# Optimization experiments

Hardware: AMD Instinct MI355X
Metric: run time of the kernel (lower is better)

## Reference

```python
import jax, jax.numpy as jnp
import numpy as np

NUM_EMBEDDINGS = 8192
EMBEDDING_DIM = 512
BETA = 0.25


def setup_inputs() -> dict:
    key = jax.random.key(0)
    k1, k2 = jax.random.split(key)
    x = jax.random.normal(k1, (16, 1024, EMBEDDING_DIM), dtype=jnp.float32)
    # torch.nn.init.uniform_ -> U[0, 1)
    embeddings = jax.random.uniform(k2, (NUM_EMBEDDINGS, EMBEDDING_DIM), dtype=jnp.float32)
    return {"x": x, "embeddings": embeddings}


def reference(x, embeddings):
    input_shape = x.shape
    flat = x.reshape(-1, EMBEDDING_DIM)                      # [N, D]
    sim = jnp.matmul(flat, embeddings.T)                     # [N, K]
    s1 = jnp.sum(flat * flat, axis=1, keepdims=True)         # [N, 1]
    s2 = jnp.sum(embeddings * embeddings, axis=1)            # [K]
    distances = s1 + s2 - 2.0 * sim                          # [N, K]
    idx = jnp.argmin(distances, axis=1)                      # [N]
    # direct gather (math-equivalent to one-hot @ codebook)
    quantized = embeddings[idx].reshape(input_shape)
    sg = jax.lax.stop_gradient
    commitment_loss = BETA * jnp.mean((sg(quantized) - x) ** 2)
    codebook_loss = jnp.mean((quantized - sg(x)) ** 2)
    loss = commitment_loss + codebook_loss
    out = x + sg(quantized - x)                              # straight-through
    return (out, quantized, loss)
```

## Files before the change

kernel.cpp:

```cpp
#include <hip/hip_runtime.h>

#define DIM 512
#define N_ROWS 16384
#define K_CODES 8192
#define BK 32
#define TM 128
#define TN 128
#define NG (K_CODES / TN)
#define OUT_ELEMS (N_ROWS * DIM)
#define MARGIN 0.125f
#define CAP_ITEMS 262144
#define NT (DIM / BK)

typedef _Float16 f16;
typedef _Float16 f16x8 __attribute__((ext_vector_type(8)));
typedef float f32x4 __attribute__((ext_vector_type(4)));

__device__ __forceinline__ unsigned long long pack_di(float d, int i) {
  unsigned u = __float_as_uint(d);
  u = (u & 0x80000000u) ? ~u : (u | 0x80000000u);
  return ((unsigned long long)u << 32) | (unsigned)i;
}

__global__ __launch_bounds__(256) void vq_split_kernel(const float* __restrict__ src,
                                                       f16* __restrict__ x16) {
  int i = (blockIdx.x * 256 + threadIdx.x) * 8;
  float4 v0 = *(const float4*)(src + i);
  float4 v1 = *(const float4*)(src + i + 4);
  float f[8] = {v0.x, v0.y, v0.z, v0.w, v1.x, v1.y, v1.z, v1.w};
  f16x8 h;
  #pragma unroll
  for (int j = 0; j < 8; ++j) h[j] = (f16)f[j];
  *(f16x8*)(x16 + i) = h;
}

__global__ __launch_bounds__(256) void vq_split_enorm_kernel(
    const float* __restrict__ emb, f16* __restrict__ e16,
    float* __restrict__ enorm, int* __restrict__ rcounter) {
  int gid  = blockIdx.x * 256 + threadIdx.x;
  if (gid == 0) *rcounter = 0;
  int code = gid >> 6;
  int lane = gid & 63;
  size_t off = (size_t)code * DIM + lane * 8;
  float4 v0 = *(const float4*)(emb + off);
  float4 v1 = *(const float4*)(emb + off + 4);
  float f[8] = {v0.x, v0.y, v0.z, v0.w, v1.x, v1.y, v1.z, v1.w};
  f16x8 h;
  float s = 0.0f;
  #pragma unroll
  for (int j = 0; j < 8; ++j) {
    h[j] = (f16)f[j];
    s = fmaf(f[j], f[j], s);
  }
  *(f16x8*)(e16 + off) = h;
  #pragma unroll
  for (int o = 32; o > 0; o >>= 1) s += __shfl_down(s, o);
  if (lane == 0) enorm[code] = s;
}

__device__ __forceinline__ void gl2lds16(const f16* g, f16* l) {
  __builtin_amdgcn_global_load_lds((const __attribute__((address_space(1))) unsigned int*)g,
                                   (__attribute__((address_space(3))) unsigned int*)l,
                                   16, 0, 0);
}

__device__ __forceinline__ void top2_merge(float& d1, int& i1, float& d2,
                                           float od1, int oi1, float od2) {
  if (od1 < d1 || (od1 == d1 && oi1 < i1)) {
    d2 = fminf(d1, od2);
    d1 = od1; i1 = oi1;
  } else {
    d2 = fminf(d2, od1);
  }
}

__global__ __launch_bounds__(256, 4) void vq_argmin_mfma_kernel(
    const f16* __restrict__ x16, const f16* __restrict__ e16,
    const float* __restrict__ enorm,
    float* __restrict__ cand_d1, int* __restrict__ cand_i1, float* __restrict__ cand_d2) {
  __shared__ __align__(16) f16 Ax[2][TM * BK];
  __shared__ __align__(16) f16 Be[2][TN * BK];
  __shared__ float red_d1[2][TM];
  __shared__ int   red_i1[2][TM];
  __shared__ float red_d2[2][TM];

  const int tid  = threadIdx.x;
  const int wave = tid >> 6;
  const int lane = tid & 63;
  const int bm = blockIdx.x, bn = blockIdx.y;
  const int wr = (wave >> 1) * 64;
  const int wc = (wave & 1) * 64;

  const f16* gsrc0;
  int ldoff;
  {
    const int srow = lane >> 2;
    const int scg  = ((lane & 3) ^ ((lane >> 3) & 3)) * 8;
    const int rowoff = (wave & 1) * 64;
    if (wave < 2) { gsrc0 = x16 + (size_t)(bm * TM + rowoff + srow) * DIM + scg; }
    else          { gsrc0 = e16 + (size_t)(bn * TN + rowoff + srow) * DIM + scg; }
    ldoff = rowoff * BK;
  }
  f16* dstA0 = (wave < 2) ? &Ax[0][ldoff] : &Be[0][ldoff];
  f16* dstA1 = (wave < 2) ? &Ax[1][ldoff] : &Be[1][ldoff];

  f32x4 acc[4][4];
  #pragma unroll
  for (int i = 0; i < 4; ++i)
    #pragma unroll
    for (int j = 0; j < 4; ++j)
      acc[i][j] = (f32x4){0.f, 0.f, 0.f, 0.f};

  const int fr = lane & 15;
  const int fq = lane >> 4;
  const int sw8 = (fq ^ ((fr >> 1) & 3)) * 8;

  #pragma unroll
  for (int i = 0; i < 4; ++i)
    gl2lds16(gsrc0 + (size_t)(16 * i) * DIM, dstA0 + (16 * i) * BK);
  __syncthreads();

  #pragma unroll 2
  for (int s = 0; s < NT; ++s) {
    const int cur = s & 1;
    if (s + 1 < NT) {
      f16* nb = cur ? dstA0 : dstA1;
      const int k1 = (s + 1) * BK;
      #pragma unroll
      for (int i = 0; i < 4; ++i)
        gl2lds16(gsrc0 + (size_t)(16 * i) * DIM + k1, nb + (16 * i) * BK);
    }

    const f16* A = cur ? &Ax[1][0] : &Ax[0][0];
    const f16* B = cur ? &Be[1][0] : &Be[0][0];
    f16x8 a[4], b[4];
    #pragma unroll
    for (int f = 0; f < 4; ++f) {
      a[f] = *(const f16x8*)&A[(wr + f * 16 + fr) * BK + sw8];
      b[f] = *(const f16x8*)&B[(wc + f * 16 + fr) * BK + sw8];
    }
    #pragma unroll
    for (int mf = 0; mf < 4; ++mf)
      #pragma unroll
      for (int nf = 0; nf < 4; ++nf)
        acc[mf][nf] = __builtin_amdgcn_mfma_f32_16x16x32_f16(a[mf], b[nf], acc[mf][nf], 0, 0, 0);

    __syncthreads();
  }

  float en[4];
  #pragma unroll
  for (int nf = 0; nf < 4; ++nf)
    en[nf] = enorm[bn * TN + wc + nf * 16 + fr];

  #pragma unroll
  for (int mf = 0; mf < 4; ++mf) {
    #pragma unroll
    for (int reg = 0; reg < 4; ++reg) {
      float d1 = 3.4e38f, d2 = 3.4e38f;
      int i1 = 0;
      #pragma unroll
      for (int nf = 0; nf < 4; ++nf) {
        float d = en[nf] - 2.0f * acc[mf][nf][reg];
        int ci = bn * TN + wc + nf * 16 + fr;
        if (d < d1) { d2 = d1; d1 = d; i1 = ci; }
        else if (d < d2) { d2 = d; }
      }
      #pragma unroll
      for (int m = 1; m <= 8; m <<= 1) {
        float od1 = __shfl_xor(d1, m, 16);
        int   oi1 = __shfl_xor(i1, m, 16);
        float od2 = __shfl_xor(d2, m, 16);
        top2_merge(d1, i1, d2, od1, oi1, od2);
      }
      if (fr == 0) {
        int row = wr + mf * 16 + fq * 4 + reg;
        red_d1[wave & 1][row] = d1;
        red_i1[wave & 1][row] = i1;
        red_d2[wave & 1][row] = d2;
      }
    }
  }
  __syncthreads();
  if (tid < TM) {
    float d1 = red_d1[0][tid]; int i1 = red_i1[0][tid]; float d2 = red_d2[0][tid];
    top2_merge(d1, i1, d2, red_d1[1][tid], red_i1[1][tid], red_d2[1][tid]);
    size_t o = (size_t)bn * N_ROWS + (size_t)bm * TM + tid;
    cand_d1[o] = d1; cand_i1[o] = i1; cand_d2[o] = d2;
  }
}

__global__ __launch_bounds__(256) void vq_merge2_kernel(
    const float* __restrict__ cd1, const int* __restrict__ ci1, const float* __restrict__ cd2,
    int* __restrict__ idx, int* __restrict__ flag,
    int* __restrict__ rcounter, int* __restrict__ item_row, int* __restrict__ item_grp,
    unsigned long long* __restrict__ packed,
    float* __restrict__ loss_slot) {
  int r = blockIdx.x * 256 + threadIdx.x;
  if (r == 0) *loss_slot = 0.0f;
  float d1 = 3.4e38f, d2 = 3.4e38f;
  int i1 = 0;
  for (int g = 0; g < NG; ++g) {
    size_t o = (size_t)g * N_ROWS + r;
    top2_merge(d1, i1, d2, cd1[o], ci1[o], cd2[o]);
  }
  idx[r] = i1;
  int f = (d2 - d1 < MARGIN) ? 1 : 0;
  flag[r] = f;
  if (f) {
    packed[r] = 0xFFFFFFFFFFFFFFFFULL;
    const float thresh = d1 + MARGIN;
    for (int g = 0; g < NG; ++g) {
      if (cd1[(size_t)g * N_ROWS + r] <= thresh) {
        int slot = atomicAdd(rcounter, 1);
        if (slot < CAP_ITEMS) { item_row[slot] = r; item_grp[slot] = g; }
      }
    }
  }
}

__global__ __launch_bounds__(128) void vq_rescan_kernel(
    const float* __restrict__ x, const float* __restrict__ emb,
    const float* __restrict__ enorm,
    const int* __restrict__ rcounter,
    const int* __restrict__ item_row, const int* __restrict__ item_grp,
    unsigned long long* __restrict__ packed) {
  __shared__ float4 xs[DIM / 4];
  __shared__ unsigned long long wred[2];
  const int t = threadIdx.x;
  int nitems = rcounter[0];
  if (nitems > CAP_ITEMS) nitems = CAP_ITEMS;
  for (int item = blockIdx.x; item < nitems; item += gridDim.x) {
    const int r = item_row[item];
    const int g = item_grp[item];
    __syncthreads();
    xs[t] = ((const float4*)(x + (size_t)r * DIM))[t];
    __syncthreads();
    const int c = g * 128 + t;
    const float4* e4 = (const float4*)(emb + (size_t)c * DIM);
    float s0 = 0.f, s1 = 0.f, s2 = 0.f, s3 = 0.f;
    for (int k = 0; k < DIM / 4; ++k) {
      float4 xv = xs[k]; float4 ev = e4[k];
      s0 = fmaf(xv.x, ev.x, s0); s1 = fmaf(xv.y, ev.y, s1);
      s2 = fmaf(xv.z, ev.z, s2); s3 = fmaf(xv.w, ev.w, s3);
    }
    float d = enorm[c] - 2.0f * ((s0 + s1) + (s2 + s3));
    unsigned long long p = pack_di(d, c);
    #pragma unroll
    for (int off = 32; off > 0; off >>= 1) {
      unsigned long long o = __shfl_down(p, off);
      if (o < p) p = o;
    }
    if ((t & 63) == 0) wred[t >> 6] = p;
    __syncthreads();
    if (t == 0) {
      unsigned long long m = wred[0];
      if (wred[1] < m) m = wred[1];
      atomicMin(&packed[r], m);
    }
  }
}

__global__ __launch_bounds__(256) void vq_gather_kernel(
    const float* __restrict__ x, const float* __restrict__ emb,
    const int* __restrict__ idx, const int* __restrict__ flag,
    const unsigned long long* __restrict__ packed,
    float* __restrict__ out, float* __restrict__ quant,
    float* __restrict__ loss_slot) {
  __shared__ float wsum[4];
  const int wave = threadIdx.x >> 6;
  const int lane = threadIdx.x & 63;
  const int row  = blockIdx.x * 4 + wave;
  const int code = flag[row] ? (int)(packed[row] & 0xFFFFFFFFu) : idx[row];
  const float4* xp = (const float4*)(x   + (size_t)row  * DIM + lane * 8);
  const float4* ep = (const float4*)(emb + (size_t)code * DIM + lane * 8);
  float s = 0.0f;
  #pragma unroll
  for (int t = 0; t < 2; ++t) {
    float4 xv = xp[t];
    float4 ev = ep[t];
    float dx = ev.x - xv.x, dy = ev.y - xv.y, dz = ev.z - xv.z, dw = ev.w - xv.w;
    s += dx * dx + dy * dy + dz * dz + dw * dw;
    ((float4*)(out   + (size_t)row * DIM + lane * 8))[t] = ev;
    ((float4*)(quant + (size_t)row * DIM + lane * 8))[t] = ev;
  }
  #pragma unroll
  for (int off = 32; off > 0; off >>= 1) s += __shfl_down(s, off);
  if (lane == 0) wsum[wave] = s;
  __syncthreads();
  if (threadIdx.x == 0) {
    float tot = wsum[0] + wsum[1] + wsum[2] + wsum[3];
    atomicAdd(loss_slot, tot * (1.25f / (float)OUT_ELEMS));
  }
}

extern "C" void kernel_launch(void* const* d_in, const int* in_sizes, int n_in,
                              void* d_out, int out_size, void* d_ws, size_t ws_size,
                              hipStream_t stream) {
  const float* x   = (const float*)d_in[0];
  const float* emb = (const float*)d_in[1];
  float* out   = (float*)d_out;
  float* quant = out + OUT_ELEMS;
  float* loss  = out + 2 * OUT_ELEMS;

  char* ws = (char*)d_ws;
  f16*   x16    = (f16*)(ws);
  f16*   e16    = (f16*)(ws + 16777216);
  float* enorm  = (float*)(ws + 25165824);
  float* cd1    = (float*)(ws + 25198592);
  int*   ci1    = (int*)  (ws + 29392896);
  float* cd2    = (float*)(ws + 33587200);
  int*   idx    = (int*)  (ws + 37781504);
  int*   flag   = (int*)  (ws + 37847040);
  int*   rcounter=(int*)  (ws + 37912576);
  unsigned long long* packed = (unsigned long long*)(ws + 37912832);
  int*   item_row=(int*)  (ws + 38043904);
  int*   item_grp=(int*)  (ws + 39092480);

  vq_split_kernel<<<OUT_ELEMS / (8 * 256), 256, 0, stream>>>(x, x16);
  vq_split_enorm_kernel<<<K_CODES * 64 / 256, 256, 0, stream>>>(emb, e16, enorm, rcounter);
  vq_argmin_mfma_kernel<<<dim3(N_ROWS / TM, K_CODES / TN), 256, 0, stream>>>(
      x16, e16, enorm, cd1, ci1, cd2);
  vq_merge2_kernel<<<N_ROWS / 256, 256, 0, stream>>>(
      cd1, ci1, cd2, idx, flag, rcounter, item_row, item_grp, packed, loss);
  vq_rescan_kernel<<<2048, 128, 0, stream>>>(
      x, emb, enorm, rcounter, item_row, item_grp, packed);
  vq_gather_kernel<<<N_ROWS / 4, 256, 0, stream>>>(x, emb, idx, flag, packed, out, quant, loss);
}
```

Measured before the change: 443.1 us.

## Enlarge argmin GEMM tile to 256 rows with 8 waves per block

Doubles the row tile of the distance/argmin MFMA kernel to 256 and launches 512 threads (8 waves), so each codebook tile loaded into LDS is reused across twice as many input rows. The global-to-LDS loads are redistributed so each wave issues three 16-row loads. Shared memory becomes one aliased buffer, with the reduction scratch overlaying the A tiles. This cuts codebook traffic per row and halves the number of blocks along M, but raises LDS use per block and may reduce occupancy.

```diff
diff --git a/kernel.cpp b/kernel.cpp
--- a/kernel.cpp
+++ b/kernel.cpp
@@ -4,7 +4,7 @@
 #define N_ROWS 16384
 #define K_CODES 8192
 #define BK 32
-#define TM 128
+#define TM 256
 #define TN 128
 #define NG (K_CODES / TN)
 #define OUT_ELEMS (N_ROWS * DIM)
@@ -74,15 +74,18 @@
   }
 }
 
-__global__ __launch_bounds__(256, 4) void vq_argmin_mfma_kernel(
+__global__ __launch_bounds__(512, 6) void vq_argmin_mfma_kernel(
     const f16* __restrict__ x16, const f16* __restrict__ e16,
     const float* __restrict__ enorm,
     float* __restrict__ cand_d1, int* __restrict__ cand_i1, float* __restrict__ cand_d2) {
-  __shared__ __align__(16) f16 Ax[2][TM * BK];
-  __shared__ __align__(16) f16 Be[2][TN * BK];
-  __shared__ float red_d1[2][TM];
-  __shared__ int   red_i1[2][TM];
-  __shared__ float red_d2[2][TM];
+  __shared__ __align__(16) char smem[49152];
+  f16* Ab0 = (f16*)smem;
+  f16* Ab1 = (f16*)(smem + 16384);
+  f16* Bb0 = (f16*)(smem + 32768);
+  f16* Bb1 = (f16*)(smem + 40960);
+  float* red_d1 = (float*)smem;
+  int*   red_i1 = (int*)(smem + 2048);
+  float* red_d2 = (float*)(smem + 4096);
 
   const int tid  = threadIdx.x;
   const int wave = tid >> 6;
@@ -91,18 +94,24 @@
   const int wr = (wave >> 1) * 64;
   const int wc = (wave & 1) * 64;
 
-  const f16* gsrc0;
-  int ldoff;
+  const int srow = lane >> 2;
+  const int scg  = ((lane & 3) ^ ((lane >> 3) & 3)) * 8;
+  const f16* gs0; const f16* gs1; const f16* gs2;
+  int doff0, doff1, doff2;
+  bool ia0, ia1, ia2;
   {
-    const int srow = lane >> 2;
-    const int scg  = ((lane & 3) ^ ((lane >> 3) & 3)) * 8;
-    const int rowoff = (wave & 1) * 64;
-    if (wave < 2) { gsrc0 = x16 + (size_t)(bm * TM + rowoff + srow) * DIM + scg; }
-    else          { gsrc0 = e16 + (size_t)(bn * TN + rowoff + srow) * DIM + scg; }
-    ldoff = rowoff * BK;
-  }
-  f16* dstA0 = (wave < 2) ? &Ax[0][ldoff] : &Be[0][ldoff];
-  f16* dstA1 = (wave < 2) ? &Ax[1][ldoff] : &Be[1][ldoff];
+    const int g0 = wave * 3, g1 = wave * 3 + 1, g2 = wave * 3 + 2;
+    ia0 = g0 < 16; ia1 = g1 < 16; ia2 = g2 < 16;
+    gs0 = ia0 ? x16 + (size_t)(bm * TM + g0 * 16 + srow) * DIM + scg
+              : e16 + (size_t)(bn * TN + (g0 - 16) * 16 + srow) * DIM + scg;
+    gs1 = ia1 ? x16 + (size_t)(bm * TM + g1 * 16 + srow) * DIM + scg
+              : e16 + (size_t)(bn * TN + (g1 - 16) * 16 + srow) * DIM + scg;
+    gs2 = ia2 ? x16 + (size_t)(bm * TM + g2 * 16 + srow) * DIM + scg
+              : e16 + (size_t)(bn * TN + (g2 - 16) * 16 + srow) * DIM + scg;
+    doff0 = (ia0 ? g0 : g0 - 16) * 16 * BK;
+    doff1 = (ia1 ? g1 : g1 - 16) * 16 * BK;
+    doff2 = (ia2 ? g2 : g2 - 16) * 16 * BK;
+  }
 
   f32x4 acc[4][4];
   #pragma unroll
@@ -115,24 +124,25 @@
   const int fq = lane >> 4;
   const int sw8 = (fq ^ ((fr >> 1) & 3)) * 8;
 
-  #pragma unroll
-  for (int i = 0; i < 4; ++i)
-    gl2lds16(gsrc0 + (size_t)(16 * i) * DIM, dstA0 + (16 * i) * BK);
+  gl2lds16(gs0, (ia0 ? Ab0 : Bb0) + doff0);
+  gl2lds16(gs1, (ia1 ? Ab0 : Bb0) + doff1);
+  gl2lds16(gs2, (ia2 ? Ab0 : Bb0) + doff2);
   __syncthreads();
 
   #pragma unroll 2
   for (int s = 0; s < NT; ++s) {
     const int cur = s & 1;
     if (s + 1 < NT) {
-      f16* nb = cur ? dstA0 : dstA1;
       const int k1 = (s + 1) * BK;
-      #pragma unroll
-      for (int i = 0; i < 4; ++i)
-        gl2lds16(gsrc0 + (size_t)(16 * i) * DIM + k1, nb + (16 * i) * BK);
-    }
-
-    const f16* A = cur ? &Ax[1][0] : &Ax[0][0];
-    const f16* B = cur ? &Be[1][0] : &Be[0][0];
+      f16* An = cur ? Ab0 : Ab1;
+      f16* Bn = cur ? Bb0 : Bb1;
+      gl2lds16(gs0 + k1, (ia0 ? An : Bn) + doff0);
+      gl2lds16(gs1 + k1, (ia1 ? An : Bn) + doff1);
+      gl2lds16(gs2 + k1, (ia2 ? An : Bn) + doff2);
+    }
+
+    const f16* A = cur ? Ab1 : Ab0;
+    const f16* B = cur ? Bb1 : Bb0;
     f16x8 a[4], b[4];
     #pragma unroll
     for (int f = 0; f < 4; ++f) {
@@ -175,16 +185,16 @@
       }
       if (fr == 0) {
         int row = wr + mf * 16 + fq * 4 + reg;
-        red_d1[wave & 1][row] = d1;
-        red_i1[wave & 1][row] = i1;
-        red_d2[wave & 1][row] = d2;
+        red_d1[(wave & 1) * TM + row] = d1;
+        red_i1[(wave & 1) * TM + row] = i1;
+        red_d2[(wave & 1) * TM + row] = d2;
       }
     }
   }
   __syncthreads();
   if (tid < TM) {
-    float d1 = red_d1[0][tid]; int i1 = red_i1[0][tid]; float d2 = red_d2[0][tid];
-    top2_merge(d1, i1, d2, red_d1[1][tid], red_i1[1][tid], red_d2[1][tid]);
+    float d1 = red_d1[tid]; int i1 = red_i1[tid]; float d2 = red_d2[tid];
+    top2_merge(d1, i1, d2, red_d1[TM + tid], red_i1[TM + tid], red_d2[TM + tid]);
     size_t o = (size_t)bn * N_ROWS + (size_t)bm * TM + tid;
     cand_d1[o] = d1; cand_i1[o] = i1; cand_d2[o] = d2;
   }
@@ -319,7 +329,7 @@
 
   vq_split_kernel<<<OUT_ELEMS / (8 * 256), 256, 0, stream>>>(x, x16);
   vq_split_enorm_kernel<<<K_CODES * 64 / 256, 256, 0, stream>>>(emb, e16, enorm, rcounter);
-  vq_argmin_mfma_kernel<<<dim3(N_ROWS / TM, K_CODES / TN), 256, 0, stream>>>(
+  vq_argmin_mfma_kernel<<<dim3(N_ROWS / TM, K_CODES / TN), 512, 0, stream>>>(
       x16, e16, enorm, cd1, ci1, cd2);
   vq_merge2_kernel<<<N_ROWS / 256, 256, 0, stream>>>(
       cd1, ci1, cd2, idx, flag, rcounter, item_row, item_grp, packed, loss);
```

After: 1.279 ms. 189% more time.
